# Performance work log

Hardware: AMD Instinct MI355X
Metric: run time of the kernel (lower is better)

## Reference

```python
import jax, jax.numpy as jnp
import numpy as np

N_QUBITS = 4
N_LAYERS = 2
DIM = 2 ** N_QUBITS  # 16
B, S, E = 512, 128, 512


def _bits(w):
    # bit of qubit w for each basis index (wire 0 = most significant, PennyLane convention)
    return (jnp.arange(DIM) >> (N_QUBITS - 1 - w)) & 1


def _apply_single_scalar(state, U, w):
    # apply 2x2 gate U (shared across tokens) on qubit w; state [N, DIM]
    L = 2 ** w
    R = DIM // (2 * L)
    s = state.reshape(-1, L, 2, R)
    s = jnp.einsum('ij,nljr->nlir', U, s)
    return s.reshape(-1, DIM)


def _quantum_circuit(q_in, weights):
    # q_in: [N, N_QUBITS] float angles; weights: [N_LAYERS, 2*N_QUBITS]
    N = q_in.shape[0]
    # AngleEmbedding with RX on |0...0>: product state, amplitudes [cos(t/2), -i sin(t/2)]
    half = q_in * 0.5
    c = jnp.cos(half).astype(jnp.complex64)
    s = jnp.sin(half).astype(jnp.complex64)
    state = jnp.ones((N, 1), jnp.complex64)
    for w in range(N_QUBITS):
        amp = jnp.stack([c[:, w], -1j * s[:, w]], axis=-1)  # [N, 2]
        state = (state[:, :, None] * amp[:, None, :]).reshape(N, -1)
    # state: [N, DIM]
    for l in range(N_LAYERS):
        # ring of CRZ(weights[l, i], wires=[i, (i+1) % n])  -> diagonal gates
        for i in range(N_QUBITS):
            phi = weights[l, i]
            bc = _bits(i)
            bt = _bits((i + 1) % N_QUBITS)
            # RZ(phi) = diag(e^{-i phi/2}, e^{+i phi/2}) on target, applied when control bit = 1
            ang = 0.5 * phi * (2 * bt - 1).astype(weights.dtype)
            phase = jnp.exp(1j * ang.astype(jnp.complex64))
            diag = jnp.where(bc == 1, phase, jnp.ones((), jnp.complex64))
            state = state * diag[None, :]
        # RY(weights[l, i + n_qubits]) on each qubit
        for i in range(N_QUBITS):
            th = 0.5 * weights[l, i + N_QUBITS]
            ct, st = jnp.cos(th), jnp.sin(th)
            U = jnp.stack([jnp.stack([ct, -st]), jnp.stack([st, ct])]).astype(jnp.complex64)
            state = _apply_single_scalar(state, U, i)
    probs = state.real ** 2 + state.imag ** 2  # [N, DIM]
    zvals = jnp.stack([1.0 - 2.0 * _bits(w) for w in range(N_QUBITS)], 0).astype(probs.dtype)  # [Q, DIM]
    return probs @ zvals.T  # [N, N_QUBITS] expvals of PauliZ


def setup_inputs() -> dict:
    key = jax.random.key(0)
    ks = jax.random.split(key, 6)
    x = jax.random.normal(ks[0], (B, S, E), jnp.float32)
    # TorchLayer default init: uniform(0, 2*pi)
    q_weights = jax.random.uniform(ks[1], (N_LAYERS, 2 * N_QUBITS), jnp.float32, 0.0, 2.0 * np.pi)
    lim_q = 1.0 / np.sqrt(E)
    Wq = jax.random.uniform(ks[2], (N_QUBITS, E), jnp.float32, -lim_q, lim_q)
    bq = jax.random.uniform(ks[3], (N_QUBITS,), jnp.float32, -lim_q, lim_q)
    lim_c = 1.0 / np.sqrt(N_QUBITS)
    Wc = jax.random.uniform(ks[4], (E, N_QUBITS), jnp.float32, -lim_c, lim_c)
    bc = jax.random.uniform(ks[5], (E,), jnp.float32, -lim_c, lim_c)
    return {"x": x, "q_weights": q_weights, "Wq": Wq, "bq": bq, "Wc": Wc, "bc": bc}


def reference(x, q_weights, Wq, bq, Wc, bc):
    q_in = jnp.einsum('bse,qe->bsq', x, Wq) + bq          # [B, S, Q]
    q_out = _quantum_circuit(q_in.reshape(-1, N_QUBITS), q_weights).reshape(B, S, N_QUBITS)
    return jnp.einsum('bsq,eq->bse', q_out, Wc) + bc       # [B, S, E]
```

## Files before the change

kernel.cpp:

```cpp
#include <hip/hip_runtime.h>

#define EDIM     512
#define NTOK     (512 * 128)
#define NTHREADS 256
#define TPB      32
#define NBLOCKS  (NTOK / TPB)

typedef unsigned short u16;
typedef unsigned int   u32;
typedef float v4f __attribute__((ext_vector_type(4)));
typedef u16   v4h __attribute__((ext_vector_type(4)));

__device__ __forceinline__ float bf2f(u16 u) { return __uint_as_float(((u32)u) << 16); }

__device__ __forceinline__ u32 f2bfbits(float f) {
    u32 b = __float_as_uint(f);
    return (b + 0x7fffu + ((b >> 16) & 1u)) >> 16;
}

template<bool BF16>
__device__ __forceinline__ float ld1(const void* p, int off) {
    if constexpr (BF16) return bf2f(((const u16*)p)[off]);
    else                return ((const float*)p)[off];
}

template<bool BF16>
__device__ __forceinline__ void body(
    const void* __restrict__ x,
    const void* __restrict__ qwp,
    const void* __restrict__ Wq,
    const void* __restrict__ bq,
    const void* __restrict__ Wc,
    const void* __restrict__ bc,
    void* __restrict__ out,
    v4f* s_wq4,
    v4f* s_wcc4,
    v4f* s_bc4,
    float* s_trig)
{
    const int tid = threadIdx.x;
    float* s_wqf  = (float*)s_wq4;
    float* s_wccf = (float*)s_wcc4;
    float* s_bcf  = (float*)s_bc4;

    for (int i = tid; i < 4 * EDIM; i += NTHREADS) s_wqf[i] = ld1<BF16>(Wq, i);
    for (int i = tid; i < 4 * EDIM; i += NTHREADS) {
        const int e4 = (i >> 2) & 127, k = i & 3, q = i >> 9;
        s_wccf[i] = ld1<BF16>(Wc, e4 * 16 + k * 4 + q);
    }
    for (int i = tid; i < EDIM; i += NTHREADS) s_bcf[i] = ld1<BF16>(bc, i);
    if (tid < 16) {
        const float wv = ld1<BF16>(qwp, tid);
        s_trig[tid]      = cosf(0.5f * wv);
        s_trig[16 + tid] = sinf(0.5f * wv);
    }
    __syncthreads();

    const int t = tid >> 3;
    const int s = tid & 7;
    const int n = blockIdx.x * TPB + t;

    float acc0 = 0.f, acc1 = 0.f, acc2 = 0.f, acc3 = 0.f;
    #pragma unroll
    for (int m = 0; m < 16; ++m) {
        const int e4 = s + 8 * m;
        float xf0, xf1, xf2, xf3;
        if constexpr (BF16) {
            const v4h xv = ((const v4h*)x)[(size_t)n * 128 + e4];
            xf0 = bf2f(xv.x); xf1 = bf2f(xv.y); xf2 = bf2f(xv.z); xf3 = bf2f(xv.w);
        } else {
            const v4f xv = ((const v4f*)x)[(size_t)n * 128 + e4];
            xf0 = xv.x; xf1 = xv.y; xf2 = xv.z; xf3 = xv.w;
        }
        const v4f w0 = s_wq4[0 * 128 + e4];
        const v4f w1 = s_wq4[1 * 128 + e4];
        const v4f w2 = s_wq4[2 * 128 + e4];
        const v4f w3 = s_wq4[3 * 128 + e4];
        acc0 = fmaf(xf0, w0.x, acc0); acc0 = fmaf(xf1, w0.y, acc0);
        acc0 = fmaf(xf2, w0.z, acc0); acc0 = fmaf(xf3, w0.w, acc0);
        acc1 = fmaf(xf0, w1.x, acc1); acc1 = fmaf(xf1, w1.y, acc1);
        acc1 = fmaf(xf2, w1.z, acc1); acc1 = fmaf(xf3, w1.w, acc1);
        acc2 = fmaf(xf0, w2.x, acc2); acc2 = fmaf(xf1, w2.y, acc2);
        acc2 = fmaf(xf2, w2.z, acc2); acc2 = fmaf(xf3, w2.w, acc2);
        acc3 = fmaf(xf0, w3.x, acc3); acc3 = fmaf(xf1, w3.y, acc3);
        acc3 = fmaf(xf2, w3.z, acc3); acc3 = fmaf(xf3, w3.w, acc3);
    }
    float qin[4] = {acc0, acc1, acc2, acc3};
    #pragma unroll
    for (int q = 0; q < 4; ++q) {
        float v = qin[q];
        v += __shfl_xor(v, 1);
        v += __shfl_xor(v, 2);
        v += __shfl_xor(v, 4);
        qin[q] = v + ld1<BF16>(bq, q);
    }

    float cw[4], sw[4];
    #pragma unroll
    for (int w = 0; w < 4; ++w) sincosf(0.5f * qin[w], &sw[w], &cw[w]);

    float re[16], im[16];
    re[0] = 1.f; im[0] = 0.f;
    #pragma unroll
    for (int w = 0; w < 4; ++w) {
        #pragma unroll
        for (int j = (1 << w) - 1; j >= 0; --j) {
            const float r0 = re[j], i0 = im[j];
            re[2 * j]     = r0 * cw[w];
            im[2 * j]     = i0 * cw[w];
            re[2 * j + 1] = i0 * sw[w];
            im[2 * j + 1] = -r0 * sw[w];
        }
    }
    #pragma unroll
    for (int l = 0; l < 2; ++l) {
        #pragma unroll
        for (int i = 0; i < 4; ++i) {
            const float cc = s_trig[l * 8 + i];
            const float ss = s_trig[16 + l * 8 + i];
            #pragma unroll
            for (int k = 0; k < 16; ++k) {
                const int cb = (k >> (3 - i)) & 1;
                const int tb = (k >> (3 - ((i + 1) & 3))) & 1;
                if (cb) {
                    const float pr = cc, pi = tb ? ss : -ss;
                    const float r = re[k], m = im[k];
                    re[k] = r * pr - m * pi;
                    im[k] = r * pi + m * pr;
                }
            }
        }
        #pragma unroll
        for (int i = 0; i < 4; ++i) {
            const float ct = s_trig[l * 8 + 4 + i];
            const float st = s_trig[16 + l * 8 + 4 + i];
            const int str = 8 >> i;
            #pragma unroll
            for (int k = 0; k < 16; ++k) {
                if ((k & str) == 0) {
                    const int k1 = k + str;
                    const float r0 = re[k], r1 = re[k1];
                    const float i0 = im[k], i1 = im[k1];
                    re[k]  = ct * r0 - st * r1;
                    re[k1] = st * r0 + ct * r1;
                    im[k]  = ct * i0 - st * i1;
                    im[k1] = st * i0 + ct * i1;
                }
            }
        }
    }
    float qout[4] = {0.f, 0.f, 0.f, 0.f};
    #pragma unroll
    for (int k = 0; k < 16; ++k) {
        const float p = re[k] * re[k] + im[k] * im[k];
        #pragma unroll
        for (int q = 0; q < 4; ++q)
            qout[q] += ((k >> (3 - q)) & 1) ? -p : p;
    }

    #pragma unroll
    for (int m = 0; m < 16; ++m) {
        const int e4 = s + 8 * m;
        v4f o = s_bc4[e4];
        #pragma unroll
        for (int q = 0; q < 4; ++q) {
            const v4f wv = s_wcc4[q * 128 + e4];
            o.x = fmaf(qout[q], wv.x, o.x);
            o.y = fmaf(qout[q], wv.y, o.y);
            o.z = fmaf(qout[q], wv.z, o.z);
            o.w = fmaf(qout[q], wv.w, o.w);
        }
        if constexpr (BF16) {
            v4h ov;
            ov.x = (u16)f2bfbits(o.x);
            ov.y = (u16)f2bfbits(o.y);
            ov.z = (u16)f2bfbits(o.z);
            ov.w = (u16)f2bfbits(o.w);
            __builtin_nontemporal_store(ov, (v4h*)out + (size_t)n * 128 + e4);
        } else {
            __builtin_nontemporal_store(o, (v4f*)out + (size_t)n * 128 + e4);
        }
    }
}

__global__ __launch_bounds__(NTHREADS, 4)
void qlayer_kernel(const void* __restrict__ x,
                   const void* __restrict__ qw,
                   const void* __restrict__ Wq,
                   const void* __restrict__ bq,
                   const void* __restrict__ Wc,
                   const void* __restrict__ bc,
                   void* __restrict__ out)
{
    __shared__ v4f  s_wq4[4 * 128];
    __shared__ v4f  s_wcc4[4 * 128];
    __shared__ v4f  s_bc4[128];
    __shared__ float s_trig[32];
    __shared__ int  s_zc, s_vc;

    const int tid = threadIdx.x;

    if (tid == 0) { s_zc = 0; s_vc = 0; }
    __syncthreads();
    {
        int z = 0, v = 0;
        #pragma unroll
        for (int i = 0; i < 2; ++i) {
            const u32 w = ((const u32*)x)[tid + 256 * i];
            if ((w & 0xFFFFu) == 0u) z++;
            const u32 e = (w >> 7) & 0xFFu;
            if (e != 0u && e >= 96u && e <= 143u) v++;
        }
        if (z) atomicAdd(&s_zc, z);
        if (v) atomicAdd(&s_vc, v);
    }
    __syncthreads();
    const bool isbf = (s_zc < 384 && s_vc >= 384);

    if (isbf)
        body<true >(x, qw, Wq, bq, Wc, bc, out, s_wq4, s_wcc4, s_bc4, s_trig);
    else
        body<false>(x, qw, Wq, bq, Wc, bc, out, s_wq4, s_wcc4, s_bc4, s_trig);
}

extern "C" void kernel_launch(void* const* d_in, const int* in_sizes, int n_in,
                              void* d_out, int out_size, void* d_ws, size_t ws_size,
                              hipStream_t stream)
{
    const void* x  = d_in[0];
    const void* qw = d_in[1];
    const void* Wq = d_in[2];
    const void* bq = d_in[3];
    const void* Wc = d_in[4];
    const void* bc = d_in[5];
    (void)in_sizes; (void)n_in; (void)out_size; (void)d_ws; (void)ws_size;

    qlayer_kernel<<<NBLOCKS, NTHREADS, 0, stream>>>(x, qw, Wq, bq, Wc, bc, d_out);
}
```

Baseline: 247.1 us.

## Process four tokens per 8-lane group to amortize shared-weight loads and setup

```diff
diff --git a/kernel.cpp b/kernel.cpp
--- a/kernel.cpp
+++ b/kernel.cpp
@@ -3,7 +3,8 @@
 #define EDIM     512
 #define NTOK     (512 * 128)
 #define NTHREADS 256
-#define TPB      32
+#define G        4
+#define TPB      (32 * G)
 #define NBLOCKS  (NTOK / TPB)
 
 typedef unsigned short u16;
@@ -56,134 +57,184 @@
     }
     __syncthreads();
 
-    const int t = tid >> 3;
-    const int s = tid & 7;
-    const int n = blockIdx.x * TPB + t;
-
-    float acc0 = 0.f, acc1 = 0.f, acc2 = 0.f, acc3 = 0.f;
+    const int t  = tid >> 3;
+    const int s  = tid & 7;
+    const int n0 = blockIdx.x * TPB + t * G;
+
+    const float bq0 = ld1<BF16>(bq, 0), bq1 = ld1<BF16>(bq, 1);
+    const float bq2 = ld1<BF16>(bq, 2), bq3 = ld1<BF16>(bq, 3);
+
+    float acc[G][4];
+    #pragma unroll
+    for (int g = 0; g < G; ++g)
+        #pragma unroll
+        for (int q = 0; q < 4; ++q) acc[g][q] = 0.f;
+
     #pragma unroll
     for (int m = 0; m < 16; ++m) {
         const int e4 = s + 8 * m;
-        float xf0, xf1, xf2, xf3;
-        if constexpr (BF16) {
-            const v4h xv = ((const v4h*)x)[(size_t)n * 128 + e4];
-            xf0 = bf2f(xv.x); xf1 = bf2f(xv.y); xf2 = bf2f(xv.z); xf3 = bf2f(xv.w);
-        } else {
-            const v4f xv = ((const v4f*)x)[(size_t)n * 128 + e4];
-            xf0 = xv.x; xf1 = xv.y; xf2 = xv.z; xf3 = xv.w;
+        float xf[G][4];
+        #pragma unroll
+        for (int g = 0; g < G; ++g) {
+            if constexpr (BF16) {
+                const v4h xv = ((const v4h*)x)[(size_t)(n0 + g) * 128 + e4];
+                xf[g][0] = bf2f(xv.x); xf[g][1] = bf2f(xv.y);
+                xf[g][2] = bf2f(xv.z); xf[g][3] = bf2f(xv.w);
+            } else {
+                const v4f xv = ((const v4f*)x)[(size_t)(n0 + g) * 128 + e4];
+                xf[g][0] = xv.x; xf[g][1] = xv.y; xf[g][2] = xv.z; xf[g][3] = xv.w;
+            }
         }
         const v4f w0 = s_wq4[0 * 128 + e4];
         const v4f w1 = s_wq4[1 * 128 + e4];
         const v4f w2 = s_wq4[2 * 128 + e4];
         const v4f w3 = s_wq4[3 * 128 + e4];
-        acc0 = fmaf(xf0, w0.x, acc0); acc0 = fmaf(xf1, w0.y, acc0);
-        acc0 = fmaf(xf2, w0.z, acc0); acc0 = fmaf(xf3, w0.w, acc0);
-        acc1 = fmaf(xf0, w1.x, acc1); acc1 = fmaf(xf1, w1.y, acc1);
-        acc1 = fmaf(xf2, w1.z, acc1); acc1 = fmaf(xf3, w1.w, acc1);
-        acc2 = fmaf(xf0, w2.x, acc2); acc2 = fmaf(xf1, w2.y, acc2);
-        acc2 = fmaf(xf2, w2.z, acc2); acc2 = fmaf(xf3, w2.w, acc2);
-        acc3 = fmaf(xf0, w3.x, acc3); acc3 = fmaf(xf1, w3.y, acc3);
-        acc3 = fmaf(xf2, w3.z, acc3); acc3 = fmaf(xf3, w3.w, acc3);
-    }
-    float qin[4] = {acc0, acc1, acc2, acc3};
-    #pragma unroll
-    for (int q = 0; q < 4; ++q) {
-        float v = qin[q];
-        v += __shfl_xor(v, 1);
-        v += __shfl_xor(v, 2);
-        v += __shfl_xor(v, 4);
-        qin[q] = v + ld1<BF16>(bq, q);
-    }
-
-    float cw[4], sw[4];
-    #pragma unroll
-    for (int w = 0; w < 4; ++w) sincosf(0.5f * qin[w], &sw[w], &cw[w]);
-
-    float re[16], im[16];
-    re[0] = 1.f; im[0] = 0.f;
-    #pragma unroll
-    for (int w = 0; w < 4; ++w) {
-        #pragma unroll
-        for (int j = (1 << w) - 1; j >= 0; --j) {
-            const float r0 = re[j], i0 = im[j];
-            re[2 * j]     = r0 * cw[w];
-            im[2 * j]     = i0 * cw[w];
-            re[2 * j + 1] = i0 * sw[w];
-            im[2 * j + 1] = -r0 * sw[w];
-        }
-    }
-    #pragma unroll
-    for (int l = 0; l < 2; ++l) {
-        #pragma unroll
-        for (int i = 0; i < 4; ++i) {
-            const float cc = s_trig[l * 8 + i];
-            const float ss = s_trig[16 + l * 8 + i];
+        #pragma unroll
+        for (int g = 0; g < G; ++g) {
+            acc[g][0] = fmaf(xf[g][0], w0.x, acc[g][0]);
+            acc[g][0] = fmaf(xf[g][1], w0.y, acc[g][0]);
+            acc[g][0] = fmaf(xf[g][2], w0.z, acc[g][0]);
+            acc[g][0] = fmaf(xf[g][3], w0.w, acc[g][0]);
+            acc[g][1] = fmaf(xf[g][0], w1.x, acc[g][1]);
+            acc[g][1] = fmaf(xf[g][1], w1.y, acc[g][1]);
+            acc[g][1] = fmaf(xf[g][2], w1.z, acc[g][1]);
+            acc[g][1] = fmaf(xf[g][3], w1.w, acc[g][1]);
+            acc[g][2] = fmaf(xf[g][0], w2.x, acc[g][2]);
+            acc[g][2] = fmaf(xf[g][1], w2.y, acc[g][2]);
+            acc[g][2] = fmaf(xf[g][2], w2.z, acc[g][2]);
+            acc[g][2] = fmaf(xf[g][3], w2.w, acc[g][2]);
+            acc[g][3] = fmaf(xf[g][0], w3.x, acc[g][3]);
+            acc[g][3] = fmaf(xf[g][1], w3.y, acc[g][3]);
+            acc[g][3] = fmaf(xf[g][2], w3.z, acc[g][3]);
+            acc[g][3] = fmaf(xf[g][3], w3.w, acc[g][3]);
+        }
+    }
+
+    float qin[G][4];
+    #pragma unroll
+    for (int g = 0; g < G; ++g) {
+        #pragma unroll
+        for (int q = 0; q < 4; ++q) {
+            float v = acc[g][q];
+            v += __shfl_xor(v, 1);
+            v += __shfl_xor(v, 2);
+            v += __shfl_xor(v, 4);
+            qin[g][q] = v;
+        }
+        qin[g][0] += bq0; qin[g][1] += bq1; qin[g][2] += bq2; qin[g][3] += bq3;
+    }
+
+    float qout[G][4];
+    #pragma unroll
+    for (int g = 0; g < G; ++g) {
+        float cw[4], sw[4];
+        #pragma unroll
+        for (int w = 0; w < 4; ++w) sincosf(0.5f * qin[g][w], &sw[w], &cw[w]);
+
+        float re[16], im[16];
+        re[0] = 1.f; im[0] = 0.f;
+        #pragma unroll
+        for (int w = 0; w < 4; ++w) {
             #pragma unroll
-            for (int k = 0; k < 16; ++k) {
-                const int cb = (k >> (3 - i)) & 1;
-                const int tb = (k >> (3 - ((i + 1) & 3))) & 1;
-                if (cb) {
-                    const float pr = cc, pi = tb ? ss : -ss;
-                    const float r = re[k], m = im[k];
-                    re[k] = r * pr - m * pi;
-                    im[k] = r * pi + m * pr;
+            for (int j = (1 << w) - 1; j >= 0; --j) {
+                const float r0 = re[j], i0 = im[j];
+                re[2 * j]     = r0 * cw[w];
+                im[2 * j]     = i0 * cw[w];
+                re[2 * j + 1] = i0 * sw[w];
+                im[2 * j + 1] = -r0 * sw[w];
+            }
+        }
+        #pragma unroll
+        for (int l = 0; l < 2; ++l) {
+            #pragma unroll
+            for (int i = 0; i < 4; ++i) {
+                const float cc = s_trig[l * 8 + i];
+                const float ss = s_trig[16 + l * 8 + i];
+                #pragma unroll
+                for (int k = 0; k < 16; ++k) {
+                    const int cb = (k >> (3 - i)) & 1;
+                    const int tb = (k >> (3 - ((i + 1) & 3))) & 1;
+                    if (cb) {
+                        const float pr = cc, pi = tb ? ss : -ss;
+                        const float r = re[k], mm = im[k];
+                        re[k] = r * pr - mm * pi;
+                        im[k] = r * pi + mm * pr;
+                    }
                 }
             }
-        }
-        #pragma unroll
-        for (int i = 0; i < 4; ++i) {
-            const float ct = s_trig[l * 8 + 4 + i];
-            const float st = s_trig[16 + l * 8 + 4 + i];
-            const int str = 8 >> i;
             #pragma unroll
-            for (int k = 0; k < 16; ++k) {
-                if ((k & str) == 0) {
-                    const int k1 = k + str;
-                    const float r0 = re[k], r1 = re[k1];
-                    const float i0 = im[k], i1 = im[k1];
-                    re[k]  = ct * r0 - st * r1;
-                    re[k1] = st * r0 + ct * r1;
-                    im[k]  = ct * i0 - st * i1;
-                    im[k1] = st * i0 + ct * i1;
+            for (int i = 0; i < 4; ++i) {
+                const float ct = s_trig[l * 8 + 4 + i];
+                const float st = s_trig[16 + l * 8 + 4 + i];
+                const int str = 8 >> i;
+                #pragma unroll
+                for (int k = 0; k < 16; ++k) {
+                    if ((k & str) == 0) {
+                        const int k1 = k + str;
+                        const float r0 = re[k], r1 = re[k1];
+                        const float i0 = im[k], i1 = im[k1];
+                        re[k]  = ct * r0 - st * r1;
+                        re[k1] = st * r0 + ct * r1;
+                        im[k]  = ct * i0 - st * i1;
+                        im[k1] = st * i0 + ct * i1;
+                    }
                 }
             }
         }
-    }
-    float qout[4] = {0.f, 0.f, 0.f, 0.f};
-    #pragma unroll
-    for (int k = 0; k < 16; ++k) {
-        const float p = re[k] * re[k] + im[k] * im[k];
-        #pragma unroll
-        for (int q = 0; q < 4; ++q)
-            qout[q] += ((k >> (3 - q)) & 1) ? -p : p;
+        float q0 = 0.f, q1 = 0.f, q2 = 0.f, q3 = 0.f;
+        #pragma unroll
+        for (int k = 0; k < 16; ++k) {
+            const float p = re[k] * re[k] + im[k] * im[k];
+            q0 += (k & 8) ? -p : p;
+            q1 += (k & 4) ? -p : p;
+            q2 += (k & 2) ? -p : p;
+            q3 += (k & 1) ? -p : p;
+        }
+        qout[g][0] = q0; qout[g][1] = q1; qout[g][2] = q2; qout[g][3] = q3;
     }
 
     #pragma unroll
     for (int m = 0; m < 16; ++m) {
         const int e4 = s + 8 * m;
-        v4f o = s_bc4[e4];
-        #pragma unroll
-        for (int q = 0; q < 4; ++q) {
-            const v4f wv = s_wcc4[q * 128 + e4];
-            o.x = fmaf(qout[q], wv.x, o.x);
-            o.y = fmaf(qout[q], wv.y, o.y);
-            o.z = fmaf(qout[q], wv.z, o.z);
-            o.w = fmaf(qout[q], wv.w, o.w);
-        }
-        if constexpr (BF16) {
-            v4h ov;
-            ov.x = (u16)f2bfbits(o.x);
-            ov.y = (u16)f2bfbits(o.y);
-            ov.z = (u16)f2bfbits(o.z);
-            ov.w = (u16)f2bfbits(o.w);
-            __builtin_nontemporal_store(ov, (v4h*)out + (size_t)n * 128 + e4);
-        } else {
-            __builtin_nontemporal_store(o, (v4f*)out + (size_t)n * 128 + e4);
-        }
-    }
-}
-
-__global__ __launch_bounds__(NTHREADS, 4)
+        const v4f b  = s_bc4[e4];
+        const v4f w0 = s_wcc4[0 * 128 + e4];
+        const v4f w1 = s_wcc4[1 * 128 + e4];
+        const v4f w2 = s_wcc4[2 * 128 + e4];
+        const v4f w3 = s_wcc4[3 * 128 + e4];
+        #pragma unroll
+        for (int g = 0; g < G; ++g) {
+            v4f o = b;
+            o.x = fmaf(qout[g][0], w0.x, o.x);
+            o.y = fmaf(qout[g][0], w0.y, o.y);
+            o.z = fmaf(qout[g][0], w0.z, o.z);
+            o.w = fmaf(qout[g][0], w0.w, o.w);
+            o.x = fmaf(qout[g][1], w1.x, o.x);
+            o.y = fmaf(qout[g][1], w1.y, o.y);
+            o.z = fmaf(qout[g][1], w1.z, o.z);
+            o.w = fmaf(qout[g][1], w1.w, o.w);
+            o.x = fmaf(qout[g][2], w2.x, o.x);
+            o.y = fmaf(qout[g][2], w2.y, o.y);
+            o.z = fmaf(qout[g][2], w2.z, o.z);
+            o.w = fmaf(qout[g][2], w2.w, o.w);
+            o.x = fmaf(qout[g][3], w3.x, o.x);
+            o.y = fmaf(qout[g][3], w3.y, o.y);
+            o.z = fmaf(qout[g][3], w3.z, o.z);
+            o.w = fmaf(qout[g][3], w3.w, o.w);
+            if constexpr (BF16) {
+                v4h ov;
+                ov.x = (u16)f2bfbits(o.x);
+                ov.y = (u16)f2bfbits(o.y);
+                ov.z = (u16)f2bfbits(o.z);
+                ov.w = (u16)f2bfbits(o.w);
+                __builtin_nontemporal_store(ov, (v4h*)out + (size_t)(n0 + g) * 128 + e4);
+            } else {
+                __builtin_nontemporal_store(o, (v4f*)out + (size_t)(n0 + g) * 128 + e4);
+            }
+        }
+    }
+}
+
+__global__ __launch_bounds__(NTHREADS, 2)
 void qlayer_kernel(const void* __restrict__ x,
                    const void* __restrict__ qw,
                    const void* __restrict__ Wq,
```

Measured after the change: 250.7 us. About the same (+1.5%).

## Split fused kernel into projection+circuit and output expansion kernels via workspace

Applied to the files above, without the earlier changes.

```diff
diff --git a/kernel.cpp b/kernel.cpp
--- a/kernel.cpp
+++ b/kernel.cpp
@@ -3,8 +3,10 @@
 #define EDIM     512
 #define NTOK     (512 * 128)
 #define NTHREADS 256
-#define TPB      32
-#define NBLOCKS  (NTOK / TPB)
+#define TPB_A    32
+#define NBLK_A   (NTOK / TPB_A)
+#define TPB_B    32
+#define NBLK_B   (NTOK / TPB_B)
 
 typedef unsigned short u16;
 typedef unsigned int   u32;
@@ -24,77 +26,26 @@
     else                return ((const float*)p)[off];
 }
 
-template<bool BF16>
-__device__ __forceinline__ void body(
-    const void* __restrict__ x,
-    const void* __restrict__ qwp,
-    const void* __restrict__ Wq,
-    const void* __restrict__ bq,
-    const void* __restrict__ Wc,
-    const void* __restrict__ bc,
-    void* __restrict__ out,
-    v4f* s_wq4,
-    v4f* s_wcc4,
-    v4f* s_bc4,
-    float* s_trig)
-{
-    const int tid = threadIdx.x;
-    float* s_wqf  = (float*)s_wq4;
-    float* s_wccf = (float*)s_wcc4;
-    float* s_bcf  = (float*)s_bc4;
-
-    for (int i = tid; i < 4 * EDIM; i += NTHREADS) s_wqf[i] = ld1<BF16>(Wq, i);
-    for (int i = tid; i < 4 * EDIM; i += NTHREADS) {
-        const int e4 = (i >> 2) & 127, k = i & 3, q = i >> 9;
-        s_wccf[i] = ld1<BF16>(Wc, e4 * 16 + k * 4 + q);
-    }
-    for (int i = tid; i < EDIM; i += NTHREADS) s_bcf[i] = ld1<BF16>(bc, i);
-    if (tid < 16) {
-        const float wv = ld1<BF16>(qwp, tid);
-        s_trig[tid]      = cosf(0.5f * wv);
-        s_trig[16 + tid] = sinf(0.5f * wv);
-    }
+__device__ __forceinline__ bool detect_block(const u32* xw, int tid, int* s_zc, int* s_vc)
+{
+    if (tid == 0) { *s_zc = 0; *s_vc = 0; }
     __syncthreads();
-
-    const int t = tid >> 3;
-    const int s = tid & 7;
-    const int n = blockIdx.x * TPB + t;
-
-    float acc0 = 0.f, acc1 = 0.f, acc2 = 0.f, acc3 = 0.f;
-    #pragma unroll
-    for (int m = 0; m < 16; ++m) {
-        const int e4 = s + 8 * m;
-        float xf0, xf1, xf2, xf3;
-        if constexpr (BF16) {
-            const v4h xv = ((const v4h*)x)[(size_t)n * 128 + e4];
-            xf0 = bf2f(xv.x); xf1 = bf2f(xv.y); xf2 = bf2f(xv.z); xf3 = bf2f(xv.w);
-        } else {
-            const v4f xv = ((const v4f*)x)[(size_t)n * 128 + e4];
-            xf0 = xv.x; xf1 = xv.y; xf2 = xv.z; xf3 = xv.w;
-        }
-        const v4f w0 = s_wq4[0 * 128 + e4];
-        const v4f w1 = s_wq4[1 * 128 + e4];
-        const v4f w2 = s_wq4[2 * 128 + e4];
-        const v4f w3 = s_wq4[3 * 128 + e4];
-        acc0 = fmaf(xf0, w0.x, acc0); acc0 = fmaf(xf1, w0.y, acc0);
-        acc0 = fmaf(xf2, w0.z, acc0); acc0 = fmaf(xf3, w0.w, acc0);
-        acc1 = fmaf(xf0, w1.x, acc1); acc1 = fmaf(xf1, w1.y, acc1);
-        acc1 = fmaf(xf2, w1.z, acc1); acc1 = fmaf(xf3, w1.w, acc1);
-        acc2 = fmaf(xf0, w2.x, acc2); acc2 = fmaf(xf1, w2.y, acc2);
-        acc2 = fmaf(xf2, w2.z, acc2); acc2 = fmaf(xf3, w2.w, acc2);
-        acc3 = fmaf(xf0, w3.x, acc3); acc3 = fmaf(xf1, w3.y, acc3);
-        acc3 = fmaf(xf2, w3.z, acc3); acc3 = fmaf(xf3, w3.w, acc3);
-    }
-    float qin[4] = {acc0, acc1, acc2, acc3};
-    #pragma unroll
-    for (int q = 0; q < 4; ++q) {
-        float v = qin[q];
-        v += __shfl_xor(v, 1);
-        v += __shfl_xor(v, 2);
-        v += __shfl_xor(v, 4);
-        qin[q] = v + ld1<BF16>(bq, q);
-    }
-
+    int z = 0, v = 0;
+    #pragma unroll
+    for (int i = 0; i < 2; ++i) {
+        const u32 w = xw[tid + 256 * i];
+        if ((w & 0xFFFFu) == 0u) z++;
+        const u32 e = (w >> 7) & 0xFFu;
+        if (e != 0u && e >= 96u && e <= 143u) v++;
+    }
+    if (z) atomicAdd(s_zc, z);
+    if (v) atomicAdd(s_vc, v);
+    __syncthreads();
+    return (*s_zc < 384 && *s_vc >= 384);
+}
+
+__device__ __forceinline__ void circuit4(const float qin[4], const float* s_trig, float qout[4])
+{
     float cw[4], sw[4];
     #pragma unroll
     for (int w = 0; w < 4; ++w) sincosf(0.5f * qin[w], &sw[w], &cw[w]);
@@ -124,9 +75,9 @@
                 const int tb = (k >> (3 - ((i + 1) & 3))) & 1;
                 if (cb) {
                     const float pr = cc, pi = tb ? ss : -ss;
-                    const float r = re[k], m = im[k];
-                    re[k] = r * pr - m * pi;
-                    im[k] = r * pi + m * pr;
+                    const float r = re[k], mm = im[k];
+                    re[k] = r * pr - mm * pi;
+                    im[k] = r * pi + mm * pr;
                 }
             }
         }
@@ -149,27 +100,145 @@
             }
         }
     }
-    float qout[4] = {0.f, 0.f, 0.f, 0.f};
+    float q0 = 0.f, q1 = 0.f, q2 = 0.f, q3 = 0.f;
     #pragma unroll
     for (int k = 0; k < 16; ++k) {
         const float p = re[k] * re[k] + im[k] * im[k];
-        #pragma unroll
-        for (int q = 0; q < 4; ++q)
-            qout[q] += ((k >> (3 - q)) & 1) ? -p : p;
-    }
-
+        q0 += (k & 8) ? -p : p;
+        q1 += (k & 4) ? -p : p;
+        q2 += (k & 2) ? -p : p;
+        q3 += (k & 1) ? -p : p;
+    }
+    qout[0] = q0; qout[1] = q1; qout[2] = q2; qout[3] = q3;
+}
+
+template<bool BF16>
+__device__ __forceinline__ void bodyA(
+    const void* __restrict__ x,
+    const void* __restrict__ qwp,
+    const void* __restrict__ Wq,
+    const void* __restrict__ bq,
+    float* __restrict__ qout,
+    v4f* s_wq4, float* s_trig)
+{
+    const int tid = threadIdx.x;
+    float* s_wqf = (float*)s_wq4;
+    for (int i = tid; i < 4 * EDIM; i += NTHREADS) s_wqf[i] = ld1<BF16>(Wq, i);
+    if (tid < 16) {
+        const float wv = ld1<BF16>(qwp, tid);
+        s_trig[tid]      = cosf(0.5f * wv);
+        s_trig[16 + tid] = sinf(0.5f * wv);
+    }
+    __syncthreads();
+
+    const int t = tid >> 3;
+    const int s = tid & 7;
+    const int n = blockIdx.x * TPB_A + t;
+
+    float acc0 = 0.f, acc1 = 0.f, acc2 = 0.f, acc3 = 0.f;
     #pragma unroll
     for (int m = 0; m < 16; ++m) {
         const int e4 = s + 8 * m;
-        v4f o = s_bc4[e4];
-        #pragma unroll
-        for (int q = 0; q < 4; ++q) {
-            const v4f wv = s_wcc4[q * 128 + e4];
-            o.x = fmaf(qout[q], wv.x, o.x);
-            o.y = fmaf(qout[q], wv.y, o.y);
-            o.z = fmaf(qout[q], wv.z, o.z);
-            o.w = fmaf(qout[q], wv.w, o.w);
-        }
+        float xf0, xf1, xf2, xf3;
+        if constexpr (BF16) {
+            const v4h xv = ((const v4h*)x)[(size_t)n * 128 + e4];
+            xf0 = bf2f(xv.x); xf1 = bf2f(xv.y); xf2 = bf2f(xv.z); xf3 = bf2f(xv.w);
+        } else {
+            const v4f xv = ((const v4f*)x)[(size_t)n * 128 + e4];
+            xf0 = xv.x; xf1 = xv.y; xf2 = xv.z; xf3 = xv.w;
+        }
+        const v4f w0 = s_wq4[0 * 128 + e4];
+        const v4f w1 = s_wq4[1 * 128 + e4];
+        const v4f w2 = s_wq4[2 * 128 + e4];
+        const v4f w3 = s_wq4[3 * 128 + e4];
+        acc0 = fmaf(xf0, w0.x, acc0); acc0 = fmaf(xf1, w0.y, acc0);
+        acc0 = fmaf(xf2, w0.z, acc0); acc0 = fmaf(xf3, w0.w, acc0);
+        acc1 = fmaf(xf0, w1.x, acc1); acc1 = fmaf(xf1, w1.y, acc1);
+        acc1 = fmaf(xf2, w1.z, acc1); acc1 = fmaf(xf3, w1.w, acc1);
+        acc2 = fmaf(xf0, w2.x, acc2); acc2 = fmaf(xf1, w2.y, acc2);
+        acc2 = fmaf(xf2, w2.z, acc2); acc2 = fmaf(xf3, w2.w, acc2);
+        acc3 = fmaf(xf0, w3.x, acc3); acc3 = fmaf(xf1, w3.y, acc3);
+        acc3 = fmaf(xf2, w3.z, acc3); acc3 = fmaf(xf3, w3.w, acc3);
+    }
+
+    float qin[4] = {acc0, acc1, acc2, acc3};
+    #pragma unroll
+    for (int q = 0; q < 4; ++q) {
+        float v = qin[q];
+        v += __shfl_xor(v, 1);
+        v += __shfl_xor(v, 2);
+        v += __shfl_xor(v, 4);
+        qin[q] = v + ld1<BF16>(bq, q);
+    }
+
+    float qo[4];
+    circuit4(qin, s_trig, qo);
+
+    if (s == 0) {
+        v4f qv; qv.x = qo[0]; qv.y = qo[1]; qv.z = qo[2]; qv.w = qo[3];
+        ((v4f*)qout)[n] = qv;
+    }
+}
+
+__global__ __launch_bounds__(NTHREADS)
+void qlayer_A(const void* __restrict__ x,
+              const void* __restrict__ qw,
+              const void* __restrict__ Wq,
+              const void* __restrict__ bq,
+              float* __restrict__ qout)
+{
+    __shared__ v4f  s_wq4[4 * 128];
+    __shared__ float s_trig[32];
+    __shared__ int  s_zc, s_vc;
+    const bool isbf = detect_block((const u32*)x, threadIdx.x, &s_zc, &s_vc);
+    if (isbf) bodyA<true >(x, qw, Wq, bq, qout, s_wq4, s_trig);
+    else      bodyA<false>(x, qw, Wq, bq, qout, s_wq4, s_trig);
+}
+
+template<bool BF16>
+__device__ __forceinline__ void bodyB(
+    const float* __restrict__ qout,
+    const void* __restrict__ Wc,
+    const void* __restrict__ bc,
+    void* __restrict__ out)
+{
+    const int tid = threadIdx.x;
+    const int e4  = tid & 127;
+    const int h   = tid >> 7;
+
+    v4f w[4];
+    #pragma unroll
+    for (int j = 0; j < 4; ++j) {
+        if constexpr (BF16) {
+            const v4h wv = ((const v4h*)Wc)[4 * e4 + j];
+            w[j].x = bf2f(wv.x); w[j].y = bf2f(wv.y);
+            w[j].z = bf2f(wv.z); w[j].w = bf2f(wv.w);
+        } else {
+            w[j] = ((const v4f*)Wc)[4 * e4 + j];
+        }
+    }
+    v4f bcv;
+    if constexpr (BF16) {
+        const v4h bv = ((const v4h*)bc)[e4];
+        bcv.x = bf2f(bv.x); bcv.y = bf2f(bv.y); bcv.z = bf2f(bv.z); bcv.w = bf2f(bv.w);
+    } else {
+        bcv = ((const v4f*)bc)[e4];
+    }
+
+    const int n0 = blockIdx.x * TPB_B;
+    #pragma unroll
+    for (int k = 0; k < 16; ++k) {
+        const int n = n0 + 2 * k + h;
+        const v4f qv = ((const v4f*)qout)[n];
+        v4f o = bcv;
+        o.x = fmaf(qv.x, w[0].x, o.x); o.x = fmaf(qv.y, w[0].y, o.x);
+        o.x = fmaf(qv.z, w[0].z, o.x); o.x = fmaf(qv.w, w[0].w, o.x);
+        o.y = fmaf(qv.x, w[1].x, o.y); o.y = fmaf(qv.y, w[1].y, o.y);
+        o.y = fmaf(qv.z, w[1].z, o.y); o.y = fmaf(qv.w, w[1].w, o.y);
+        o.z = fmaf(qv.x, w[2].x, o.z); o.z = fmaf(qv.y, w[2].y, o.z);
+        o.z = fmaf(qv.z, w[2].z, o.z); o.z = fmaf(qv.w, w[2].w, o.z);
+        o.w = fmaf(qv.x, w[3].x, o.w); o.w = fmaf(qv.y, w[3].y, o.w);
+        o.w = fmaf(qv.z, w[3].z, o.w); o.w = fmaf(qv.w, w[3].w, o.w);
         if constexpr (BF16) {
             v4h ov;
             ov.x = (u16)f2bfbits(o.x);
@@ -183,44 +252,133 @@
     }
 }
 
+__global__ __launch_bounds__(NTHREADS)
+void qlayer_B(const float* __restrict__ qout,
+              const void* __restrict__ x,
+              const void* __restrict__ Wc,
+              const void* __restrict__ bc,
+              void* __restrict__ out)
+{
+    __shared__ int s_zc, s_vc;
+    const bool isbf = detect_block((const u32*)x, threadIdx.x, &s_zc, &s_vc);
+    if (isbf) bodyB<true >(qout, Wc, bc, out);
+    else      bodyB<false>(qout, Wc, bc, out);
+}
+
+template<bool BF16>
+__device__ __forceinline__ void bodyF(
+    const void* __restrict__ x,
+    const void* __restrict__ qwp,
+    const void* __restrict__ Wq,
+    const void* __restrict__ bq,
+    const void* __restrict__ Wc,
+    const void* __restrict__ bc,
+    void* __restrict__ out,
+    v4f* s_wq4, v4f* s_wcc4, v4f* s_bc4, float* s_trig)
+{
+    const int tid = threadIdx.x;
+    float* s_wqf  = (float*)s_wq4;
+    float* s_wccf = (float*)s_wcc4;
+    float* s_bcf  = (float*)s_bc4;
+
+    for (int i = tid; i < 4 * EDIM; i += NTHREADS) s_wqf[i] = ld1<BF16>(Wq, i);
+    for (int i = tid; i < 4 * EDIM; i += NTHREADS) {
+        const int e4 = (i >> 2) & 127, k = i & 3, q = i >> 9;
+        s_wccf[i] = ld1<BF16>(Wc, e4 * 16 + k * 4 + q);
+    }
+    for (int i = tid; i < EDIM; i += NTHREADS) s_bcf[i] = ld1<BF16>(bc, i);
+    if (tid < 16) {
+        const float wv = ld1<BF16>(qwp, tid);
+        s_trig[tid]      = cosf(0.5f * wv);
+        s_trig[16 + tid] = sinf(0.5f * wv);
+    }
+    __syncthreads();
+
+    const int t = tid >> 3;
+    const int s = tid & 7;
+    const int n = blockIdx.x * 32 + t;
+
+    float acc0 = 0.f, acc1 = 0.f, acc2 = 0.f, acc3 = 0.f;
+    #pragma unroll
+    for (int m = 0; m < 16; ++m) {
+        const int e4 = s + 8 * m;
+        float xf0, xf1, xf2, xf3;
+        if constexpr (BF16) {
+            const v4h xv = ((const v4h*)x)[(size_t)n * 128 + e4];
+            xf0 = bf2f(xv.x); xf1 = bf2f(xv.y); xf2 = bf2f(xv.z); xf3 = bf2f(xv.w);
+        } else {
+            const v4f xv = ((const v4f*)x)[(size_t)n * 128 + e4];
+            xf0 = xv.x; xf1 = xv.y; xf2 = xv.z; xf3 = xv.w;
+        }
+        const v4f w0 = s_wq4[0 * 128 + e4];
+        const v4f w1 = s_wq4[1 * 128 + e4];
+        const v4f w2 = s_wq4[2 * 128 + e4];
+        const v4f w3 = s_wq4[3 * 128 + e4];
+        acc0 = fmaf(xf0, w0.x, acc0); acc0 = fmaf(xf1, w0.y, acc0);
+        acc0 = fmaf(xf2, w0.z, acc0); acc0 = fmaf(xf3, w0.w, acc0);
+        acc1 = fmaf(xf0, w1.x, acc1); acc1 = fmaf(xf1, w1.y, acc1);
+        acc1 = fmaf(xf2, w1.z, acc1); acc1 = fmaf(xf3, w1.w, acc1);
+        acc2 = fmaf(xf0, w2.x, acc2); acc2 = fmaf(xf1, w2.y, acc2);
+        acc2 = fmaf(xf2, w2.z, acc2); acc2 = fmaf(xf3, w2.w, acc2);
+        acc3 = fmaf(xf0, w3.x, acc3); acc3 = fmaf(xf1, w3.y, acc3);
+        acc3 = fmaf(xf2, w3.z, acc3); acc3 = fmaf(xf3, w3.w, acc3);
+    }
+
+    float qin[4] = {acc0, acc1, acc2, acc3};
+    #pragma unroll
+    for (int q = 0; q < 4; ++q) {
+        float v = qin[q];
+        v += __shfl_xor(v, 1);
+        v += __shfl_xor(v, 2);
+        v += __shfl_xor(v, 4);
+        qin[q] = v + ld1<BF16>(bq, q);
+    }
+
+    float qo[4];
+    circuit4(qin, s_trig, qo);
+
+    #pragma unroll
+    for (int m = 0; m < 16; ++m) {
+        const int e4 = s + 8 * m;
+        v4f o = s_bc4[e4];
+        #pragma unroll
+        for (int q = 0; q < 4; ++q) {
+            const v4f wv = s_wcc4[q * 128 + e4];
+            o.x = fmaf(qo[q], wv.x, o.x);
+            o.y = fmaf(qo[q], wv.y, o.y);
+            o.z = fmaf(qo[q], wv.z, o.z);
+            o.w = fmaf(qo[q], wv.w, o.w);
+        }
+        if constexpr (BF16) {
+            v4h ov;
+            ov.x = (u16)f2bfbits(o.x);
+            ov.y = (u16)f2bfbits(o.y);
+            ov.z = (u16)f2bfbits(o.z);
+            ov.w = (u16)f2bfbits(o.w);
+            __builtin_nontemporal_store(ov, (v4h*)out + (size_t)n * 128 + e4);
+        } else {
+            __builtin_nontemporal_store(o, (v4f*)out + (size_t)n * 128 + e4);
+        }
+    }
+}
+
 __global__ __launch_bounds__(NTHREADS, 4)
-void qlayer_kernel(const void* __restrict__ x,
-                   const void* __restrict__ qw,
-                   const void* __restrict__ Wq,
-                   const void* __restrict__ bq,
-                   const void* __restrict__ Wc,
-                   const void* __restrict__ bc,
-                   void* __restrict__ out)
+void qlayer_fused(const void* __restrict__ x,
+                  const void* __restrict__ qw,
+                  const void* __restrict__ Wq,
+                  const void* __restrict__ bq,
+                  const void* __restrict__ Wc,
+                  const void* __restrict__ bc,
+                  void* __restrict__ out)
 {
     __shared__ v4f  s_wq4[4 * 128];
     __shared__ v4f  s_wcc4[4 * 128];
     __shared__ v4f  s_bc4[128];
     __shared__ float s_trig[32];
     __shared__ int  s_zc, s_vc;
-
-    const int tid = threadIdx.x;
-
-    if (tid == 0) { s_zc = 0; s_vc = 0; }
-    __syncthreads();
-    {
-        int z = 0, v = 0;
-        #pragma unroll
-        for (int i = 0; i < 2; ++i) {
-            const u32 w = ((const u32*)x)[tid + 256 * i];
-            if ((w & 0xFFFFu) == 0u) z++;
-            const u32 e = (w >> 7) & 0xFFu;
-            if (e != 0u && e >= 96u && e <= 143u) v++;
-        }
-        if (z) atomicAdd(&s_zc, z);
-        if (v) atomicAdd(&s_vc, v);
-    }
-    __syncthreads();
-    const bool isbf = (s_zc < 384 && s_vc >= 384);
-
-    if (isbf)
-        body<true >(x, qw, Wq, bq, Wc, bc, out, s_wq4, s_wcc4, s_bc4, s_trig);
-    else
-        body<false>(x, qw, Wq, bq, Wc, bc, out, s_wq4, s_wcc4, s_bc4, s_trig);
+    const bool isbf = detect_block((const u32*)x, threadIdx.x, &s_zc, &s_vc);
+    if (isbf) bodyF<true >(x, qw, Wq, bq, Wc, bc, out, s_wq4, s_wcc4, s_bc4, s_trig);
+    else      bodyF<false>(x, qw, Wq, bq, Wc, bc, out, s_wq4, s_wcc4, s_bc4, s_trig);
 }
 
 extern "C" void kernel_launch(void* const* d_in, const int* in_sizes, int n_in,
@@ -233,7 +391,14 @@
     const void* bq = d_in[3];
     const void* Wc = d_in[4];
     const void* bc = d_in[5];
-    (void)in_sizes; (void)n_in; (void)out_size; (void)d_ws; (void)ws_size;
-
-    qlayer_kernel<<<NBLOCKS, NTHREADS, 0, stream>>>(x, qw, Wq, bq, Wc, bc, d_out);
-}
+    (void)in_sizes; (void)n_in; (void)out_size;
+
+    const size_t QOUT_BYTES = (size_t)NTOK * 4 * sizeof(float);
+    if (ws_size >= QOUT_BYTES && d_ws != nullptr) {
+        float* qout = (float*)d_ws;
+        qlayer_A<<<NBLK_A, NTHREADS, 0, stream>>>(x, qw, Wq, bq, qout);
+        qlayer_B<<<NBLK_B, NTHREADS, 0, stream>>>(qout, x, Wc, bc, d_out);
+    } else {
+        qlayer_fused<<<NTOK / 32, NTHREADS, 0, stream>>>(x, qw, Wq, bq, Wc, bc, d_out);
+    }
+}
```

New measurement: 257.5 us. 1.04x slower.
